# Kernel tuning notes

Measured on AMD Instinct MI355X. Metric: run time of the kernel, lower is better.

## Reference

```python
import jax, jax.numpy as jnp
import numpy as np

B, S, E = 8, 2048, 256
NQ = 10
FF = 1024


def _cnot(state, c, t, n):
    # state: [T, 2^n]; wire 0 is the most-significant bit.
    T = state.shape[0]
    s = state.reshape((T,) + (2,) * n)
    ctrl0 = jnp.take(s, 0, axis=c + 1)
    ctrl1 = jnp.take(s, 1, axis=c + 1)
    # target axis index after removing the control axis
    t_ax = t + 1 if (t + 1) < (c + 1) else t
    ctrl1 = jnp.flip(ctrl1, axis=t_ax)  # X on target where control==1
    s = jnp.stack([ctrl0, ctrl1], axis=c + 1)
    return s.reshape(T, -1)


def _quantum_layer(tok, theta, n):
    # tok: [T, E] real; uses first n features as RX angles. Returns [T, n] PauliZ expvals.
    T = tok.shape[0]
    half = tok[:, :n] * 0.5
    c = jnp.cos(half).astype(jnp.complex64)
    s = (-1j * jnp.sin(half)).astype(jnp.complex64)
    # RX(theta)|0> = cos(t/2)|0> - i sin(t/2)|1>; build product state wire-by-wire
    state = jnp.ones((T, 1), dtype=jnp.complex64)
    for w in range(n):
        qb = jnp.stack([c[:, w], s[:, w]], axis=1)  # [T, 2]
        state = (state[:, :, None] * qb[:, None, :]).reshape(T, -1)
    # trainable RY per wire
    th = theta * 0.5
    for w in range(n):
        ct, st = jnp.cos(th[w]), jnp.sin(th[w])
        U = jnp.stack([jnp.stack([ct, -st]), jnp.stack([st, ct])]).astype(jnp.complex64)
        sr = state.reshape(T, 2 ** w, 2, -1)
        state = jnp.einsum('ij,tajb->taib', U, sr).reshape(T, -1)
    # CNOT ring
    for cw in range(n - 1):
        state = _cnot(state, cw, cw + 1, n)
    state = _cnot(state, n - 1, 0, n)
    probs = state.real ** 2 + state.imag ** 2  # [T, 2^n]
    idx = jnp.arange(2 ** n)
    bits = (idx[None, :] >> (n - 1 - jnp.arange(n)[:, None])) & 1  # [n, 2^n]
    z = (1.0 - 2.0 * bits).astype(probs.dtype)
    return probs @ z.T  # [T, n]


def setup_inputs() -> dict:
    key = jax.random.key(0)
    ks = jax.random.split(key, 6)
    return {
        'x': jax.random.normal(ks[0], (B, S, E), dtype=jnp.float32),
        'theta': jax.random.normal(ks[1], (NQ,), dtype=jnp.float32),
        'w1': jax.random.normal(ks[2], (FF, NQ), dtype=jnp.float32) * (1.0 / np.sqrt(NQ)),
        'b1': jax.random.normal(ks[3], (FF,), dtype=jnp.float32) * 0.02,
        'w2': jax.random.normal(ks[4], (E, FF), dtype=jnp.float32) * (1.0 / np.sqrt(FF)),
        'b2': jax.random.normal(ks[5], (E,), dtype=jnp.float32) * 0.02,
    }


def reference(x, theta, w1, b1, w2, b2):
    b, s, e = x.shape
    n = theta.shape[0]
    q = _quantum_layer(x.reshape(b * s, e), theta, n).reshape(b, s, n)
    # dropout is identity in eval mode
    h = jax.nn.relu(q @ w1.T + b1)
    return h @ w2.T + b2
```

## Files before the change

kernel.cpp:

```cpp
#include <hip/hip_runtime.h>
#include <math.h>

typedef __attribute__((ext_vector_type(8))) short bf16x8;
typedef __attribute__((ext_vector_type(4))) float f32x4;

#define T_TOT 16384
#define E_ 256
#define FF_ 1024
#define NQ 10
#define TB 64
#define CH 256
#define NCHUNK (FF_ / CH)

__device__ __forceinline__ unsigned short f2bf(float f) {
    unsigned u = __builtin_bit_cast(unsigned, f);
    u = (u + 0x7FFFu + ((u >> 16) & 1u)) >> 16;
    return (unsigned short)u;
}

__global__ __launch_bounds__(256) void ffq_prep(
    const float* __restrict__ w2, const float* __restrict__ w1,
    uint4* __restrict__ w2f, uint4* __restrict__ w1f)
{
    int id = blockIdx.x * 256 + threadIdx.x;
    if (id < 32768) {
        int l = id & 63, nt = (id >> 6) & 15, kk = id >> 10;
        int n  = nt * 16 + (l & 15);
        int k0 = kk * 32 + (l >> 4) * 8;
        const float4* s = (const float4*)(w2 + (size_t)n * FF_ + k0);
        float4 a = s[0], b = s[1];
        uint4 v;
        v.x = f2bf(a.x) | ((unsigned)f2bf(a.y) << 16);
        v.y = f2bf(a.z) | ((unsigned)f2bf(a.w) << 16);
        v.z = f2bf(b.x) | ((unsigned)f2bf(b.y) << 16);
        v.w = f2bf(b.z) | ((unsigned)f2bf(b.w) << 16);
        w2f[id] = v;
    } else if (id < 32768 + 4096) {
        int id2 = id - 32768;
        int l = id2 & 63, nt = id2 >> 6;
        int n = nt * 16 + (l & 15);
        int g = l >> 4;
        unsigned short o[8];
#pragma unroll
        for (int j = 0; j < 8; ++j) {
            int k = g * 8 + j;
            o[j] = (k < NQ) ? f2bf(w1[n * NQ + k]) : (unsigned short)0;
        }
        uint4 v;
        v.x = o[0] | ((unsigned)o[1] << 16);
        v.y = o[2] | ((unsigned)o[3] << 16);
        v.z = o[4] | ((unsigned)o[5] << 16);
        v.w = o[6] | ((unsigned)o[7] << 16);
        w1f[id2] = v;
    }
}

__global__ __launch_bounds__(512, 4) void ffq_mfma(
    const float* __restrict__ x, const float* __restrict__ theta,
    const float* __restrict__ b1, const float* __restrict__ b2,
    const bf16x8* __restrict__ w1f, const bf16x8* __restrict__ w2f,
    float* __restrict__ out)
{
    __shared__ unsigned short q_s[4 * 64 * 8];
    __shared__ unsigned short hs[TB * CH];

    const int tid  = threadIdx.x;
    const int l    = tid & 63;
    const int wv   = tid >> 6;
    const int lr   = l & 15;
    const int g    = l >> 4;
    const int chb  = blockIdx.x & 1;
    const int tb   = (blockIdx.x >> 1) * TB;
    const int ncol = chb * 8 + wv;

    if (tid < TB) {
        const int t = tb + tid;
        float xv[NQ];
        {
            float4 a = *(const float4*)(x + (size_t)t * E_);
            float4 b = *(const float4*)(x + (size_t)t * E_ + 4);
            float2 c = *(const float2*)(x + (size_t)t * E_ + 8);
            xv[0]=a.x; xv[1]=a.y; xv[2]=a.z; xv[3]=a.w;
            xv[4]=b.x; xv[5]=b.y; xv[6]=b.z; xv[7]=b.w;
            xv[8]=c.x; xv[9]=c.y;
        }
        float mm[NQ];
#pragma unroll
        for (int w = 0; w < NQ; ++w) mm[w] = cosf(theta[w]) * cosf(xv[w]);
        float qv[NQ];
        {
            float p = mm[0];
#pragma unroll
            for (int w = 1; w < NQ; ++w) { p *= mm[w]; qv[w] = p; }
            float p0 = mm[1];
#pragma unroll
            for (int w = 2; w < NQ; ++w) p0 *= mm[w];
            qv[0] = p0;
        }
        unsigned short qb[10];
#pragma unroll
        for (int k = 0; k < NQ; ++k) qb[k] = f2bf(qv[k]);
        uint4 s0, s1;
        s0.x = qb[0] | ((unsigned)qb[1] << 16);
        s0.y = qb[2] | ((unsigned)qb[3] << 16);
        s0.z = qb[4] | ((unsigned)qb[5] << 16);
        s0.w = qb[6] | ((unsigned)qb[7] << 16);
        s1.x = qb[8] | ((unsigned)qb[9] << 16);
        s1.y = 0; s1.z = 0; s1.w = 0;
        int tt = tid >> 4, r = tid & 15;
        uint4* base = (uint4*)q_s + tt * 64;
        base[r]      = s0;
        base[16 + r] = s1;
        base[32 + r] = make_uint4(0, 0, 0, 0);
        base[48 + r] = make_uint4(0, 0, 0, 0);
    }
    __syncthreads();

    bf16x8 qf[4];
#pragma unroll
    for (int tt = 0; tt < 4; ++tt) qf[tt] = ((const bf16x8*)q_s)[tt * 64 + l];

    f32x4 acc[4];
#pragma unroll
    for (int tt = 0; tt < 4; ++tt) acc[tt] = (f32x4){0.f, 0.f, 0.f, 0.f};

    bf16x8 bcur = w2f[(0 * 16 + ncol) * 64 + l];

    for (int c = 0; c < NCHUNK; ++c) {
#pragma unroll
        for (int fi = 0; fi < 2; ++fi) {
            const int ftl = wv * 2 + fi;
            const int ntg = c * 16 + ftl;
            bf16x8 wf = w1f[ntg * 64 + l];
            const int f0 = ntg * 16 + g * 4;
            float4 bb = *(const float4*)(b1 + f0);
            const int fl = ftl * 16 + g * 4;
            const int s  = (fl & 31) >> 3;
            const int gran = (fl >> 5) * 64 + lr + 16 * s;
#pragma unroll
            for (int tt = 0; tt < 4; ++tt) {
                f32x4 d = {0.f, 0.f, 0.f, 0.f};
                d = __builtin_amdgcn_mfma_f32_16x16x32_bf16(wf, qf[tt], d, 0, 0, 0);
                unsigned p0 = f2bf(fmaxf(d[0] + bb.x, 0.f))
                            | ((unsigned)f2bf(fmaxf(d[1] + bb.y, 0.f)) << 16);
                unsigned p1 = f2bf(fmaxf(d[2] + bb.z, 0.f))
                            | ((unsigned)f2bf(fmaxf(d[3] + bb.w, 0.f)) << 16);
                unsigned byteoff = (unsigned)(tt * 512 + gran) * 16u
                                 + (unsigned)(fl & 7) * 2u;
                *(uint2*)((char*)hs + byteoff) = make_uint2(p0, p1);
            }
        }
        __syncthreads();

#pragma unroll
        for (int kkl = 0; kkl < 8; ++kkl) {
            const int kk  = c * 8 + kkl;
            const int kkn = (kk + 1 < 32) ? kk + 1 : 31;
            bf16x8 bnext = w2f[(kkn * 16 + ncol) * 64 + l];
            bf16x8 af[4];
#pragma unroll
            for (int tt = 0; tt < 4; ++tt)
                af[tt] = ((const bf16x8*)hs)[(tt * 8 + kkl) * 64 + l];
#pragma unroll
            for (int tt = 0; tt < 4; ++tt)
                acc[tt] = __builtin_amdgcn_mfma_f32_16x16x32_bf16(
                    af[tt], bcur, acc[tt], 0, 0, 0);
            bcur = bnext;
        }
        __syncthreads();
    }

    {
        const int col = ncol * 16 + lr;
        const float bbv = b2[col];
#pragma unroll
        for (int tt = 0; tt < 4; ++tt) {
#pragma unroll
            for (int r = 0; r < 4; ++r) {
                int tr = tb + tt * 16 + g * 4 + r;
                out[(size_t)tr * E_ + col] = acc[tt][r] + bbv;
            }
        }
    }
}

extern "C" void kernel_launch(void* const* d_in, const int* in_sizes, int n_in,
                              void* d_out, int out_size, void* d_ws, size_t ws_size,
                              hipStream_t stream) {
    const float* x     = (const float*)d_in[0];
    const float* theta = (const float*)d_in[1];
    const float* w1    = (const float*)d_in[2];
    const float* b1    = (const float*)d_in[3];
    const float* w2    = (const float*)d_in[4];
    const float* b2    = (const float*)d_in[5];
    float* out = (float*)d_out;

    uint4* w2f = (uint4*)d_ws;
    uint4* w1f = (uint4*)((char*)d_ws + 512 * 1024);

    hipLaunchKernelGGL(ffq_prep, dim3(144), dim3(256), 0, stream,
                       w2, w1, w2f, w1f);
    hipLaunchKernelGGL(ffq_mfma, dim3(2 * T_TOT / TB), dim3(512), 0, stream,
                       x, theta, b1, b2,
                       (const bf16x8*)w1f, (const bf16x8*)w2f, out);
}
```

Measured before the change: 28.26 us.

## Double-buffer hidden activations in LDS and coalesce w2 prep reads

The per-chunk hidden-activation tile in shared memory is now double-buffered. The next chunk's first GEMM plus ReLU is computed after the current chunk's second GEMM, which removes one __syncthreads per chunk and lets the phases overlap. The w1 fragments for the next chunk are prefetched early. The w2 prep kernel now reads rows contiguously and scatters into the fragment layout instead of gathering. LDS use doubles to 64 KB of hidden buffer, which may reduce blocks per CU.

```diff
diff --git a/kernel.cpp b/kernel.cpp
--- a/kernel.cpp
+++ b/kernel.cpp
@@ -11,6 +11,7 @@
 #define TB 64
 #define CH 256
 #define NCHUNK (FF_ / CH)
+#define HGRAN (TB * CH)
 
 __device__ __forceinline__ unsigned short f2bf(float f) {
     unsigned u = __builtin_bit_cast(unsigned, f);
@@ -24,9 +25,8 @@
 {
     int id = blockIdx.x * 256 + threadIdx.x;
     if (id < 32768) {
-        int l = id & 63, nt = (id >> 6) & 15, kk = id >> 10;
-        int n  = nt * 16 + (l & 15);
-        int k0 = kk * 32 + (l >> 4) * 8;
+        int n  = id >> 7;
+        int k0 = (id & 127) * 8;
         const float4* s = (const float4*)(w2 + (size_t)n * FF_ + k0);
         float4 a = s[0], b = s[1];
         uint4 v;
@@ -34,7 +34,8 @@
         v.y = f2bf(a.z) | ((unsigned)f2bf(a.w) << 16);
         v.z = f2bf(b.x) | ((unsigned)f2bf(b.y) << 16);
         v.w = f2bf(b.z) | ((unsigned)f2bf(b.w) << 16);
-        w2f[id] = v;
+        int idx = ((k0 >> 5) * 16 + (n >> 4)) * 64 + ((k0 >> 3) & 3) * 16 + (n & 15);
+        w2f[idx] = v;
     } else if (id < 32768 + 4096) {
         int id2 = id - 32768;
         int l = id2 & 63, nt = id2 >> 6;
@@ -62,7 +63,7 @@
     float* __restrict__ out)
 {
     __shared__ unsigned short q_s[4 * 64 * 8];
-    __shared__ unsigned short hs[TB * CH];
+    __shared__ unsigned short hs[2 * HGRAN];
 
     const int tid  = threadIdx.x;
     const int l    = tid & 63;
@@ -124,33 +125,51 @@
 #pragma unroll
     for (int tt = 0; tt < 4; ++tt) acc[tt] = (f32x4){0.f, 0.f, 0.f, 0.f};
 
+#define H_PHASE(cc, hdst, wfa)                                                 \
+    {                                                                          \
+        _Pragma("unroll")                                                      \
+        for (int fi = 0; fi < 2; ++fi) {                                       \
+            const int ftl = wv * 2 + fi;                                       \
+            const int ntg = (cc) * 16 + ftl;                                   \
+            const int f0  = ntg * 16 + g * 4;                                  \
+            float4 bb = *(const float4*)(b1 + f0);                             \
+            const int fl   = ftl * 16 + g * 4;                                 \
+            const int sl   = (fl & 31) >> 3;                                   \
+            const int gran = (fl >> 5) * 64 + lr + 16 * sl;                    \
+            _Pragma("unroll")                                                  \
+            for (int tt = 0; tt < 4; ++tt) {                                   \
+                f32x4 d = {0.f, 0.f, 0.f, 0.f};                                \
+                d = __builtin_amdgcn_mfma_f32_16x16x32_bf16(                   \
+                        (wfa)[fi], qf[tt], d, 0, 0, 0);                        \
+                unsigned p0 = f2bf(fmaxf(d[0] + bb.x, 0.f))                    \
+                            | ((unsigned)f2bf(fmaxf(d[1] + bb.y, 0.f)) << 16); \
+                unsigned p1 = f2bf(fmaxf(d[2] + bb.z, 0.f))                    \
+                            | ((unsigned)f2bf(fmaxf(d[3] + bb.w, 0.f)) << 16); \
+                unsigned byteoff = (unsigned)(tt * 512 + gran) * 16u           \
+                                 + (unsigned)(fl & 7) * 2u;                    \
+                *(uint2*)((char*)(hdst) + byteoff) = make_uint2(p0, p1);       \
+            }                                                                  \
+        }                                                                      \
+    }
+
+    {
+        bf16x8 wf0[2];
+        wf0[0] = w1f[(0 * 16 + wv * 2 + 0) * 64 + l];
+        wf0[1] = w1f[(0 * 16 + wv * 2 + 1) * 64 + l];
+        H_PHASE(0, hs, wf0)
+    }
     bf16x8 bcur = w2f[(0 * 16 + ncol) * 64 + l];
+    __syncthreads();
 
     for (int c = 0; c < NCHUNK; ++c) {
-#pragma unroll
-        for (int fi = 0; fi < 2; ++fi) {
-            const int ftl = wv * 2 + fi;
-            const int ntg = c * 16 + ftl;
-            bf16x8 wf = w1f[ntg * 64 + l];
-            const int f0 = ntg * 16 + g * 4;
-            float4 bb = *(const float4*)(b1 + f0);
-            const int fl = ftl * 16 + g * 4;
-            const int s  = (fl & 31) >> 3;
-            const int gran = (fl >> 5) * 64 + lr + 16 * s;
-#pragma unroll
-            for (int tt = 0; tt < 4; ++tt) {
-                f32x4 d = {0.f, 0.f, 0.f, 0.f};
-                d = __builtin_amdgcn_mfma_f32_16x16x32_bf16(wf, qf[tt], d, 0, 0, 0);
-                unsigned p0 = f2bf(fmaxf(d[0] + bb.x, 0.f))
-                            | ((unsigned)f2bf(fmaxf(d[1] + bb.y, 0.f)) << 16);
-                unsigned p1 = f2bf(fmaxf(d[2] + bb.z, 0.f))
-                            | ((unsigned)f2bf(fmaxf(d[3] + bb.w, 0.f)) << 16);
-                unsigned byteoff = (unsigned)(tt * 512 + gran) * 16u
-                                 + (unsigned)(fl & 7) * 2u;
-                *(uint2*)((char*)hs + byteoff) = make_uint2(p0, p1);
-            }
-        }
-        __syncthreads();
+        const int cur = c & 1;
+        const unsigned short* hcur = hs + cur * HGRAN;
+        unsigned short*       hnxt = hs + (cur ^ 1) * HGRAN;
+
+        const int cn = (c < NCHUNK - 1) ? c + 1 : NCHUNK - 1;
+        bf16x8 wfn[2];
+        wfn[0] = w1f[(cn * 16 + wv * 2 + 0) * 64 + l];
+        wfn[1] = w1f[(cn * 16 + wv * 2 + 1) * 64 + l];
 
 #pragma unroll
         for (int kkl = 0; kkl < 8; ++kkl) {
@@ -160,15 +179,20 @@
             bf16x8 af[4];
 #pragma unroll
             for (int tt = 0; tt < 4; ++tt)
-                af[tt] = ((const bf16x8*)hs)[(tt * 8 + kkl) * 64 + l];
+                af[tt] = ((const bf16x8*)hcur)[(tt * 8 + kkl) * 64 + l];
 #pragma unroll
             for (int tt = 0; tt < 4; ++tt)
                 acc[tt] = __builtin_amdgcn_mfma_f32_16x16x32_bf16(
                     af[tt], bcur, acc[tt], 0, 0, 0);
             bcur = bnext;
         }
+
+        if (c < NCHUNK - 1) {
+            H_PHASE(c + 1, hnxt, wfn)
+        }
         __syncthreads();
     }
+#undef H_PHASE
 
     {
         const int col = ncol * 16 + lr;
```

New measurement: 27.06 us. -4.2%, faster.
